# Kernel tuning notes

Hardware: AMD Instinct MI355X
Metric: run time of the kernel (lower is better)

Reference implementation:

```python
import jax, jax.numpy as jnp
import numpy as np

N_NODES = 50000
N_EDGES = 800000


def setup_inputs() -> dict:
    key = jax.random.key(0)
    ks = jax.random.split(key, 9)
    d, h, hd = 128, 4, 32
    s = 1.0 / np.sqrt(d)
    return {
        "x": jax.random.normal(ks[0], (N_NODES, d), jnp.float32),
        "edge_index": jax.random.randint(ks[1], (2, N_EDGES), 0, N_NODES, jnp.int32),
        "W0": jax.random.normal(ks[2], (d, d), jnp.float32) * s,
        "att_l0": jax.random.normal(ks[3], (h, hd), jnp.float32) * s,
        "att_r0": jax.random.normal(ks[4], (h, hd), jnp.float32) * s,
        "b0": jnp.zeros((d,), jnp.float32),
        "W1": jax.random.normal(ks[5], (d, d), jnp.float32) * s,
        "att_l1": jax.random.normal(ks[6], (h, hd), jnp.float32) * s,
        "att_r1": jax.random.normal(ks[7], (h, hd), jnp.float32) * s,
        "b1": jnp.zeros((hd,), jnp.float32),
    }


def _gat_layer(x, src, dst, W, att_l, att_r, bias, concat):
    # x: [N, F_in]; W: [H*D, F_in] (torch Linear layout); att_*: [H, D]
    n = x.shape[0]
    h, d = att_l.shape
    hx = (x @ W.T).reshape(n, h, d)                     # [N,H,D]
    al = jnp.einsum('nhd,hd->nh', hx, att_l)            # [N,H]
    ar = jnp.einsum('nhd,hd->nh', hx, att_r)
    att = al[src] + ar[dst]                             # [E,H]
    att = jax.nn.leaky_relu(att, negative_slope=0.2)
    # segment softmax over destination nodes
    m = jax.ops.segment_max(att, dst, num_segments=n)   # [N,H]
    att = jnp.exp(att - m[dst])
    ssum = jax.ops.segment_sum(att, dst, num_segments=n)
    att = att / (ssum[dst] + 1e-9)                      # [E,H]
    msgs = att[:, :, None] * hx[src]                    # [E,H,D]
    out = jax.ops.segment_sum(msgs, dst, num_segments=n)  # [N,H,D]
    if concat:
        out = out.reshape(n, h * d)
    else:
        out = out.mean(axis=1)
    return out + bias


def reference(x, edge_index, W0, att_l0, att_r0, b0, W1, att_l1, att_r1, b1):
    src, dst = edge_index[0], edge_index[1]
    x = _gat_layer(x, src, dst, W0, att_l0, att_r0, b0, concat=True)
    x = jax.nn.relu(x)  # dropout is identity in eval mode
    x = _gat_layer(x, src, dst, W1, att_l1, att_r1, b1, concat=False)
    return x
```

## Files before the change

### kernel.cpp

```cpp
#include <hip/hip_runtime.h>
#include <hip/hip_bf16.h>

#define H 4
#define D 32
#define F 128
#define MAXDEG 64
#define PF 16
#define NBUCK 256
#define BUCKW 196
#define CAP   4096
#define NABLK 128
#define GB    1563

typedef __attribute__((ext_vector_type(8))) short bf16x8;
typedef __attribute__((ext_vector_type(4))) float f32x4;

__device__ __forceinline__ short f2bf(float v) {
    __hip_bfloat16 h = __float2bfloat16(v);
    return *reinterpret_cast<short*>(&h);
}
__device__ __forceinline__ float bf2f(short s) {
    __hip_bfloat16 h = *reinterpret_cast<__hip_bfloat16*>(&s);
    return __bfloat162float(h);
}

__global__ __launch_bounds__(256)
void k_init(const float* __restrict__ W0, short* __restrict__ W0hi,
            short* __restrict__ W0lo, const float* __restrict__ W1,
            short* __restrict__ W1hi, short* __restrict__ W1lo,
            int* __restrict__ gcnt) {
    const int bid = blockIdx.x;
    const int tid = threadIdx.x;
    if (bid == 0) gcnt[tid] = 0;
    const float* W  = (bid < 4) ? W0 : W1;
    short* Whi = (bid < 4) ? W0hi : W1hi;
    short* Wlo = (bid < 4) ? W0lo : W1lo;
    const int part = bid & 3;
    const int base = part * (F * F / 4);
    for (int i = base + tid * 4; i < base + F * F / 4; i += 1024) {
        float4 v = *reinterpret_cast<const float4*>(W + i);
        float vv[4] = {v.x, v.y, v.z, v.w};
        short hs[4], ls[4];
#pragma unroll
        for (int j = 0; j < 4; ++j) {
            hs[j] = f2bf(vv[j]);
            ls[j] = f2bf(vv[j] - bf2f(hs[j]));
        }
        *reinterpret_cast<short4*>(Whi + i) = make_short4(hs[0], hs[1], hs[2], hs[3]);
        *reinterpret_cast<short4*>(Wlo + i) = make_short4(ls[0], ls[1], ls[2], ls[3]);
    }
}

__device__ __forceinline__
void bucketA_body(int abid, const int* __restrict__ ei, int E,
                  int* __restrict__ gcnt, unsigned int* __restrict__ buf) {
    __shared__ int lcnt[NBUCK];
    __shared__ int lpos[NBUCK];
    const int tid = threadIdx.x;
    lcnt[tid] = 0;
    __syncthreads();
    const int per = ((E / NABLK) + 3) & ~3;
    const int e0 = abid * per;
    const int e1 = min(e0 + per, E);
    for (int e = e0 + 4 * tid; e < e1; e += 1024) {
        int4 dv = *reinterpret_cast<const int4*>(ei + E + e);
        atomicAdd(&lcnt[dv.x / BUCKW], 1);
        atomicAdd(&lcnt[dv.y / BUCKW], 1);
        atomicAdd(&lcnt[dv.z / BUCKW], 1);
        atomicAdd(&lcnt[dv.w / BUCKW], 1);
    }
    __syncthreads();
    if (lcnt[tid] > 0)
        lpos[tid] = atomicAdd(&gcnt[tid], lcnt[tid]);
    __syncthreads();
    for (int e = e0 + 4 * tid; e < e1; e += 1024) {
        int4 sv = *reinterpret_cast<const int4*>(ei + e);
        int4 dv = *reinterpret_cast<const int4*>(ei + E + e);
        int ss[4] = {sv.x, sv.y, sv.z, sv.w};
        int dd[4] = {dv.x, dv.y, dv.z, dv.w};
#pragma unroll
        for (int j = 0; j < 4; ++j) {
            int b = dd[j] / BUCKW;
            int pos = atomicAdd(&lpos[b], 1);
            if (pos < CAP)
                buf[(size_t)b * CAP + pos] =
                    (unsigned)ss[j] | ((unsigned)(dd[j] - b * BUCKW) << 16);
        }
    }
}

__device__ __forceinline__
void bsetup_pre(const short* __restrict__ Whi, const short* __restrict__ Wlo,
                int wave, int m, int q8, bf16x8 Bhi[2][4], bf16x8 Blo[2][4]) {
#pragma unroll
    for (int j = 0; j < 2; ++j) {
        const int fout = wave * 32 + j * 16 + m;
#pragma unroll
        for (int kc = 0; kc < 4; ++kc) {
            Bhi[j][kc] = *reinterpret_cast<const bf16x8*>(Whi + (size_t)fout * F + kc * 32 + q8);
            Blo[j][kc] = *reinterpret_cast<const bf16x8*>(Wlo + (size_t)fout * F + kc * 32 + q8);
        }
    }
}

__device__ __forceinline__
void loadA_f32(const float* __restrict__ X, int node0, int m, int q8, float4 r[8]) {
    const float* xp = X + (size_t)(node0 + m) * F + q8;
#pragma unroll
    for (int kc = 0; kc < 4; ++kc) {
        r[2 * kc]     = *reinterpret_cast<const float4*>(xp + kc * 32);
        r[2 * kc + 1] = *reinterpret_cast<const float4*>(xp + kc * 32 + 4);
    }
}

__device__ __forceinline__
void splitA(const float4 r[8], bf16x8 Ahi[4], bf16x8 Alo[4]) {
#pragma unroll
    for (int kc = 0; kc < 4; ++kc) {
        float xv[8] = {r[2 * kc].x, r[2 * kc].y, r[2 * kc].z, r[2 * kc].w,
                       r[2 * kc + 1].x, r[2 * kc + 1].y, r[2 * kc + 1].z, r[2 * kc + 1].w};
#pragma unroll
        for (int t2 = 0; t2 < 8; ++t2) {
            short hh = f2bf(xv[t2]);
            Ahi[kc][t2] = hh;
            Alo[kc][t2] = f2bf(xv[t2] - bf2f(hh));
        }
    }
}

__device__ __forceinline__
void loadA_bf(const short* __restrict__ Xhi, const short* __restrict__ Xlo,
              int node0, int m, int q8, bf16x8 Ahi[4], bf16x8 Alo[4]) {
    const short* xh = Xhi + (size_t)(node0 + m) * F + q8;
    const short* xl = Xlo + (size_t)(node0 + m) * F + q8;
#pragma unroll
    for (int kc = 0; kc < 4; ++kc) {
        Ahi[kc] = *reinterpret_cast<const bf16x8*>(xh + kc * 32);
        Alo[kc] = *reinterpret_cast<const bf16x8*>(xl + kc * 32);
    }
}

__device__ __forceinline__
void mfma_epi(int tile, const bf16x8 Ahi[4], const bf16x8 Alo[4],
              const bf16x8 Bhi[2][4], const bf16x8 Blo[2][4],
              float alw0, float alw16, float arw0, float arw16,
              __hip_bfloat16* __restrict__ HXB, float* __restrict__ AL,
              float* __restrict__ AR, int wave, int m, int q) {
    const int node0 = tile * 16;
    f32x4 acc0 = {0.f, 0.f, 0.f, 0.f};
    f32x4 acc1 = {0.f, 0.f, 0.f, 0.f};
#pragma unroll
    for (int kc = 0; kc < 4; ++kc) {
        acc0 = __builtin_amdgcn_mfma_f32_16x16x32_bf16(Ahi[kc], Bhi[0][kc], acc0, 0, 0, 0);
        acc1 = __builtin_amdgcn_mfma_f32_16x16x32_bf16(Ahi[kc], Bhi[1][kc], acc1, 0, 0, 0);
        acc0 = __builtin_amdgcn_mfma_f32_16x16x32_bf16(Ahi[kc], Blo[0][kc], acc0, 0, 0, 0);
        acc1 = __builtin_amdgcn_mfma_f32_16x16x32_bf16(Ahi[kc], Blo[1][kc], acc1, 0, 0, 0);
        acc0 = __builtin_amdgcn_mfma_f32_16x16x32_bf16(Alo[kc], Bhi[0][kc], acc0, 0, 0, 0);
        acc1 = __builtin_amdgcn_mfma_f32_16x16x32_bf16(Alo[kc], Bhi[1][kc], acc1, 0, 0, 0);
    }
    const int row0 = node0 + q * 4;
    const int col0 = wave * 32 + m;
#pragma unroll
    for (int r = 0; r < 4; ++r) {
        HXB[(size_t)(row0 + r) * F + col0]      = __float2bfloat16(acc0[r]);
        HXB[(size_t)(row0 + r) * F + col0 + 16] = __float2bfloat16(acc1[r]);
        float pal = acc0[r] * alw0 + acc1[r] * alw16;
        float par = acc0[r] * arw0 + acc1[r] * arw16;
#pragma unroll
        for (int o = 1; o < 16; o <<= 1) {
            pal += __shfl_xor(pal, o);
            par += __shfl_xor(par, o);
        }
        if (m == 0) {
            AL[(size_t)(row0 + r) * H + wave] = pal;
            AR[(size_t)(row0 + r) * H + wave] = par;
        }
    }
}

__device__ __forceinline__
void gemm_pair_f32(int bid, const float* __restrict__ X,
                   const short* __restrict__ Whi, const short* __restrict__ Wlo,
                   const float* __restrict__ attl, const float* __restrict__ attr,
                   __hip_bfloat16* __restrict__ HXB, float* __restrict__ AL,
                   float* __restrict__ AR, int ntiles) {
    const int wave = threadIdx.x >> 6;
    const int lane = threadIdx.x & 63;
    const int m    = lane & 15;
    const int q    = lane >> 4;
    const int q8   = q * 8;
    bf16x8 Bhi[2][4], Blo[2][4];
    bsetup_pre(Whi, Wlo, wave, m, q8, Bhi, Blo);
    const float alw0  = attl[wave * 32 + m];
    const float alw16 = attl[wave * 32 + 16 + m];
    const float arw0  = attr[wave * 32 + m];
    const float arw16 = attr[wave * 32 + 16 + m];

    const int t0 = bid, t1 = bid + GB;
    const bool has1 = t1 < ntiles;
    float4 r0[8], r1[8];
    loadA_f32(X, t0 * 16, m, q8, r0);
    if (has1) loadA_f32(X, t1 * 16, m, q8, r1);
    bf16x8 Ahi[4], Alo[4];
    splitA(r0, Ahi, Alo);
    mfma_epi(t0, Ahi, Alo, Bhi, Blo, alw0, alw16, arw0, arw16, HXB, AL, AR, wave, m, q);
    if (has1) {
        splitA(r1, Ahi, Alo);
        mfma_epi(t1, Ahi, Alo, Bhi, Blo, alw0, alw16, arw0, arw16, HXB, AL, AR, wave, m, q);
    }
}

__device__ __forceinline__
void gemm_pair_bf(int bid, const short* __restrict__ Xhi, const short* __restrict__ Xlo,
                  const short* __restrict__ Whi, const short* __restrict__ Wlo,
                  const float* __restrict__ attl, const float* __restrict__ attr,
                  __hip_bfloat16* __restrict__ HXB, float* __restrict__ AL,
                  float* __restrict__ AR, int ntiles) {
    const int wave = threadIdx.x >> 6;
    const int lane = threadIdx.x & 63;
    const int m    = lane & 15;
    const int q    = lane >> 4;
    const int q8   = q * 8;
    bf16x8 Bhi[2][4], Blo[2][4];
    bsetup_pre(Whi, Wlo, wave, m, q8, Bhi, Blo);
    const float alw0  = attl[wave * 32 + m];
    const float alw16 = attl[wave * 32 + 16 + m];
    const float arw0  = attr[wave * 32 + m];
    const float arw16 = attr[wave * 32 + 16 + m];

    const int t0 = bid, t1 = bid + GB;
    const bool has1 = t1 < ntiles;
    bf16x8 A0h[4], A0l[4], A1h[4], A1l[4];
    loadA_bf(Xhi, Xlo, t0 * 16, m, q8, A0h, A0l);
    if (has1) loadA_bf(Xhi, Xlo, t1 * 16, m, q8, A1h, A1l);
    mfma_epi(t0, A0h, A0l, Bhi, Blo, alw0, alw16, arw0, arw16, HXB, AL, AR, wave, m, q);
    if (has1)
        mfma_epi(t1, A1h, A1l, Bhi, Blo, alw0, alw16, arw0, arw16, HXB, AL, AR, wave, m, q);
}

__global__ __launch_bounds__(256)
void k_pre(const float* __restrict__ X, const short* __restrict__ W0hi,
           const short* __restrict__ W0lo, const float* __restrict__ attl0,
           const float* __restrict__ attr0, __hip_bfloat16* __restrict__ HXB,
           float* __restrict__ AL, float* __restrict__ AR, int ntiles,
           const int* __restrict__ ei, int E,
           int* __restrict__ gcnt, unsigned int* __restrict__ buf) {
    const int bid = blockIdx.x;
    if (bid < GB)
        gemm_pair_f32(bid, X, W0hi, W0lo, attl0, attr0, HXB, AL, AR, ntiles);
    else
        bucketA_body(bid - GB, ei, E, gcnt, buf);
}

__global__ __launch_bounds__(256)
void k_bucket(const unsigned int* __restrict__ buf, const int* __restrict__ gcnt,
              int* __restrict__ deg, unsigned short* __restrict__ ssrc2u, int N) {
    __shared__ int cnt[BUCKW];
    __shared__ unsigned short slots[BUCKW * MAXDEG];
    const int b = blockIdx.x;
    const int tid = threadIdx.x;
    if (tid < BUCKW) cnt[tid] = 0;
    __syncthreads();
    const int mm = min(gcnt[b], CAP);
    const int m4 = mm & ~3;
    for (int i = 4 * tid; i < m4; i += 1024) {
        uint4 r = *reinterpret_cast<const uint4*>(buf + (size_t)b * CAP + i);
        unsigned rr[4] = {r.x, r.y, r.z, r.w};
#pragma unroll
        for (int j = 0; j < 4; ++j) {
            int src  = rr[j] & 0xffff;
            int ldst = rr[j] >> 16;
            int slot = atomicAdd(&cnt[ldst], 1);
            if (slot < MAXDEG)
                slots[ldst * MAXDEG + slot] = (unsigned short)src;
        }
    }
    for (int i = m4 + tid; i < mm; i += 256) {
        unsigned rec = buf[(size_t)b * CAP + i];
        int src  = rec & 0xffff;
        int ldst = rec >> 16;
        int slot = atomicAdd(&cnt[ldst], 1);
        if (slot < MAXDEG)
            slots[ldst * MAXDEG + slot] = (unsigned short)src;
    }
    __syncthreads();
    uint4* dst = reinterpret_cast<uint4*>(ssrc2u + (size_t)b * BUCKW * MAXDEG);
    const uint4* s4 = reinterpret_cast<const uint4*>(slots);
    for (int i = tid; i < BUCKW * MAXDEG / 8; i += 256)
        dst[i] = s4[i];
    if (tid < BUCKW) {
        int node = b * BUCKW + tid;
        if (node < N) deg[node] = cnt[tid];
    }
}

__device__ __forceinline__
int stage_node(int g, int t, int n, const unsigned short* __restrict__ ssrc2u,
               const int* __restrict__ deg, const float* __restrict__ AL,
               const float4 ar4, int (*sidx)[MAXDEG], float (*sw)[MAXDEG][H]) {
    const int cnt  = min(deg[n], MAXDEG);
    const int rcnt = (cnt + PF - 1) & ~(PF - 1);
    if (t < rcnt) {
        if (t < cnt) {
            int s = ssrc2u[(size_t)n * MAXDEG + t];
            sidx[g][t] = s;
            float4 al4 = *reinterpret_cast<const float4*>(AL + (size_t)s * H);
            float a0 = al4.x + ar4.x; a0 = a0 > 0.f ? a0 : 0.2f * a0;
            float a1 = al4.y + ar4.y; a1 = a1 > 0.f ? a1 : 0.2f * a1;
            float a2 = al4.z + ar4.z; a2 = a2 > 0.f ? a2 : 0.2f * a2;
            float a3 = al4.w + ar4.w; a3 = a3 > 0.f ? a3 : 0.2f * a3;
            sw[g][t][0] = __expf(a0);
            sw[g][t][1] = __expf(a1);
            sw[g][t][2] = __expf(a2);
            sw[g][t][3] = __expf(a3);
        } else {
            sidx[g][t] = 0;
            sw[g][t][0] = 0.f; sw[g][t][1] = 0.f; sw[g][t][2] = 0.f; sw[g][t][3] = 0.f;
        }
    }
    __builtin_amdgcn_wave_barrier();
    return rcnt;
}

__device__ __forceinline__
void gather_node(int g, int t, int h, int rcnt, const __hip_bfloat16* __restrict__ HXB,
                 const int (*sidx)[MAXDEG], const float (*sw)[MAXDEG][H],
                 float& accx, float& accy, float& wsum) {
    for (int base = 0; base < rcnt; base += PF) {
        __hip_bfloat162 v[PF];
#pragma unroll
        for (int j = 0; j < PF; ++j) {
            int s = sidx[g][base + j];
            v[j] = *reinterpret_cast<const __hip_bfloat162*>(HXB + (size_t)s * F + 2 * t);
        }
#pragma unroll
        for (int j = 0; j < PF; ++j) {
            float w = sw[g][base + j][h];
            float2 f = __bfloat1622float2(v[j]);
            accx += w * f.x;
            accy += w * f.y;
            wsum += w;
        }
    }
}

__global__ __launch_bounds__(256)
void k_aggr0(const unsigned short* __restrict__ ssrc2u, const int* __restrict__ deg,
             const float* __restrict__ AL, const float* __restrict__ AR,
             const __hip_bfloat16* __restrict__ HXB, const float* __restrict__ bias,
             short* __restrict__ X1hi, short* __restrict__ X1lo, int N) {
    __shared__ int   sidx[4][MAXDEG];
    __shared__ float sw[4][MAXDEG][H];
    const int g = threadIdx.x >> 6;
    const int t = threadIdx.x & 63;
    const int n = blockIdx.x * 4 + g;
    if (n >= N) return;
    const int h = t >> 4;
    const float4 ar4 = *reinterpret_cast<const float4*>(AR + (size_t)n * H);
    int rcnt = stage_node(g, t, n, ssrc2u, deg, AL, ar4, sidx, sw);
    float accx = 0.f, accy = 0.f, wsum = 0.f;
    gather_node(g, t, h, rcnt, HXB, sidx, sw, accx, accy, wsum);
    float inv = 1.f / (wsum + 1e-9f);
    float ox = fmaxf(accx * inv + bias[2 * t], 0.f);
    float oy = fmaxf(accy * inv + bias[2 * t + 1], 0.f);
    short h0 = f2bf(ox), h1 = f2bf(oy);
    short l0 = f2bf(ox - bf2f(h0)), l1 = f2bf(oy - bf2f(h1));
    unsigned hw = (unsigned)(unsigned short)h0 | ((unsigned)(unsigned short)h1 << 16);
    unsigned lw = (unsigned)(unsigned short)l0 | ((unsigned)(unsigned short)l1 << 16);
    *reinterpret_cast<unsigned*>(X1hi + (size_t)n * F + 2 * t) = hw;
    *reinterpret_cast<unsigned*>(X1lo + (size_t)n * F + 2 * t) = lw;
}

__global__ __launch_bounds__(256)
void k_gemm1(const short* __restrict__ X1hi, const short* __restrict__ X1lo,
             const short* __restrict__ W1hi, const short* __restrict__ W1lo,
             const float* __restrict__ attl, const float* __restrict__ attr,
             __hip_bfloat16* __restrict__ HXB, float* __restrict__ AL,
             float* __restrict__ AR, int ntiles) {
    gemm_pair_bf(blockIdx.x, X1hi, X1lo, W1hi, W1lo, attl, attr,
                 HXB, AL, AR, ntiles);
}

__global__ __launch_bounds__(256)
void k_aggr1(const unsigned short* __restrict__ ssrc2u, const int* __restrict__ deg,
             const float* __restrict__ AL, const float* __restrict__ AR,
             const __hip_bfloat16* __restrict__ HXB, const float* __restrict__ bias,
             float* __restrict__ out, int N) {
    __shared__ int   sidx[4][MAXDEG];
    __shared__ float sw[4][MAXDEG][H];
    const int g = threadIdx.x >> 6;
    const int t = threadIdx.x & 63;
    const int n = blockIdx.x * 4 + g;
    if (n >= N) return;
    const int h = t >> 4;
    const float4 ar4 = *reinterpret_cast<const float4*>(AR + (size_t)n * H);
    int rcnt = stage_node(g, t, n, ssrc2u, deg, AL, ar4, sidx, sw);
    float accx = 0.f, accy = 0.f, wsum = 0.f;
    gather_node(g, t, h, rcnt, HXB, sidx, sw, accx, accy, wsum);
    float inv = 1.f / (wsum + 1e-9f);
    float vx = accx * inv, vy = accy * inv;
    vx += __shfl_xor(vx, 16); vx += __shfl_xor(vx, 32);
    vy += __shfl_xor(vy, 16); vy += __shfl_xor(vy, 32);
    if (t < 16) {
        float2 o;
        o.x = 0.25f * vx + bias[2 * t];
        o.y = 0.25f * vy + bias[2 * t + 1];
        *reinterpret_cast<float2*>(out + (size_t)n * D + 2 * t) = o;
    }
}

extern "C" void kernel_launch(void* const* d_in, const int* in_sizes, int n_in,
                              void* d_out, int out_size, void* d_ws, size_t ws_size,
                              hipStream_t stream) {
    const float* x     = (const float*)d_in[0];
    const int*   ei    = (const int*)d_in[1];
    const float* W0    = (const float*)d_in[2];
    const float* attl0 = (const float*)d_in[3];
    const float* attr0 = (const float*)d_in[4];
    const float* b0    = (const float*)d_in[5];
    const float* W1    = (const float*)d_in[6];
    const float* attl1 = (const float*)d_in[7];
    const float* attr1 = (const float*)d_in[8];
    const float* b1    = (const float*)d_in[9];

    const int N = in_sizes[0] / F;
    const int E = in_sizes[1] / 2;
    const int ntiles = N / 16;

    char* p = (char*)d_ws;
    __hip_bfloat16* HXB = (__hip_bfloat16*)p;   p += (size_t)N * F * 2;
    short* X1hi = (short*)p;                    p += (size_t)N * F * 2;
    short* X1lo = (short*)p;                    p += (size_t)N * F * 2;
    short* W0hi = (short*)p;                    p += (size_t)F * F * 2;
    short* W0lo = (short*)p;                    p += (size_t)F * F * 2;
    short* W1hi = (short*)p;                    p += (size_t)F * F * 2;
    short* W1lo = (short*)p;                    p += (size_t)F * F * 2;
    float* AL   = (float*)p;                    p += (size_t)N * H * 4;
    float* AR   = (float*)p;                    p += (size_t)N * H * 4;
    unsigned short* ssrc2u = (unsigned short*)p;
    p += (size_t)NBUCK * BUCKW * MAXDEG * 2;
    int* deg = (int*)p;                         p += (size_t)N * 4;
    unsigned int* buf = (unsigned int*)p;       p += (size_t)NBUCK * CAP * 4;
    int* gcnt = (int*)p;

    k_init<<<8, 256, 0, stream>>>(W0, W0hi, W0lo, W1, W1hi, W1lo, gcnt);

    k_pre<<<GB + NABLK, 256, 0, stream>>>(x, W0hi, W0lo, attl0, attr0,
                                          HXB, AL, AR, ntiles, ei, E, gcnt, buf);

    k_bucket<<<NBUCK, 256, 0, stream>>>(buf, gcnt, deg, ssrc2u, N);

    k_aggr0<<<(N + 3) / 4, 256, 0, stream>>>(ssrc2u, deg, AL, AR, HXB, b0,
                                             X1hi, X1lo, N);

    k_gemm1<<<GB, 256, 0, stream>>>(X1hi, X1lo, W1hi, W1lo, attl1, attr1,
                                    HXB, AL, AR, ntiles);

    k_aggr1<<<(N + 3) / 4, 256, 0, stream>>>(ssrc2u, deg, AL, AR, HXB, b1,
                                             (float*)d_out, N);
}
```

Measured before the change: 222.9 us.

## Replace global-atomic bucket offsets with per-block fixed-size segments and count matrix

Each bucketing block now writes its edges into a private fixed-capacity segment per bucket and records its per-bucket count in a count matrix, instead of reserving ranges with global atomics on a shared counter. The bucket kernel reads the count matrix and walks the 128 segments, so the counter no longer has to be zeroed in the init kernel. This removes global atomic contention and the init dependency. Segments are padded to 16-byte chunks, which adds reads of unused slots, and a block that sends more than 64 edges to one bucket silently drops the excess.

```diff
diff --git a/kernel.cpp b/kernel.cpp
--- a/kernel.cpp
+++ b/kernel.cpp
@@ -8,8 +8,8 @@
 #define PF 16
 #define NBUCK 256
 #define BUCKW 196
-#define CAP   4096
 #define NABLK 128
+#define SEGCAP 64
 #define GB    1563
 
 typedef __attribute__((ext_vector_type(8))) short bf16x8;
@@ -27,11 +27,9 @@
 __global__ __launch_bounds__(256)
 void k_init(const float* __restrict__ W0, short* __restrict__ W0hi,
             short* __restrict__ W0lo, const float* __restrict__ W1,
-            short* __restrict__ W1hi, short* __restrict__ W1lo,
-            int* __restrict__ gcnt) {
+            short* __restrict__ W1hi, short* __restrict__ W1lo) {
     const int bid = blockIdx.x;
     const int tid = threadIdx.x;
-    if (bid == 0) gcnt[tid] = 0;
     const float* W  = (bid < 4) ? W0 : W1;
     short* Whi = (bid < 4) ? W0hi : W1hi;
     short* Wlo = (bid < 4) ? W0lo : W1lo;
@@ -53,9 +51,8 @@
 
 __device__ __forceinline__
 void bucketA_body(int abid, const int* __restrict__ ei, int E,
-                  int* __restrict__ gcnt, unsigned int* __restrict__ buf) {
+                  int* __restrict__ cntmat, unsigned int* __restrict__ buf) {
     __shared__ int lcnt[NBUCK];
-    __shared__ int lpos[NBUCK];
     const int tid = threadIdx.x;
     lcnt[tid] = 0;
     __syncthreads();
@@ -70,8 +67,8 @@
         atomicAdd(&lcnt[dv.w / BUCKW], 1);
     }
     __syncthreads();
-    if (lcnt[tid] > 0)
-        lpos[tid] = atomicAdd(&gcnt[tid], lcnt[tid]);
+    cntmat[abid * NBUCK + tid] = min(lcnt[tid], SEGCAP);
+    lcnt[tid] = 0;
     __syncthreads();
     for (int e = e0 + 4 * tid; e < e1; e += 1024) {
         int4 sv = *reinterpret_cast<const int4*>(ei + e);
@@ -81,9 +78,9 @@
 #pragma unroll
         for (int j = 0; j < 4; ++j) {
             int b = dd[j] / BUCKW;
-            int pos = atomicAdd(&lpos[b], 1);
-            if (pos < CAP)
-                buf[(size_t)b * CAP + pos] =
+            int pos = atomicAdd(&lcnt[b], 1);
+            if (pos < SEGCAP)
+                buf[((size_t)b * NABLK + abid) * SEGCAP + pos] =
                     (unsigned)ss[j] | ((unsigned)(dd[j] - b * BUCKW) << 16);
         }
     }
@@ -244,44 +241,42 @@
            const float* __restrict__ attr0, __hip_bfloat16* __restrict__ HXB,
            float* __restrict__ AL, float* __restrict__ AR, int ntiles,
            const int* __restrict__ ei, int E,
-           int* __restrict__ gcnt, unsigned int* __restrict__ buf) {
+           int* __restrict__ cntmat, unsigned int* __restrict__ buf) {
     const int bid = blockIdx.x;
     if (bid < GB)
         gemm_pair_f32(bid, X, W0hi, W0lo, attl0, attr0, HXB, AL, AR, ntiles);
     else
-        bucketA_body(bid - GB, ei, E, gcnt, buf);
-}
-
-__global__ __launch_bounds__(256)
-void k_bucket(const unsigned int* __restrict__ buf, const int* __restrict__ gcnt,
+        bucketA_body(bid - GB, ei, E, cntmat, buf);
+}
+
+__global__ __launch_bounds__(256)
+void k_bucket(const unsigned int* __restrict__ buf, const int* __restrict__ cntmat,
               int* __restrict__ deg, unsigned short* __restrict__ ssrc2u, int N) {
     __shared__ int cnt[BUCKW];
+    __shared__ int scnt[NABLK];
     __shared__ unsigned short slots[BUCKW * MAXDEG];
     const int b = blockIdx.x;
     const int tid = threadIdx.x;
     if (tid < BUCKW) cnt[tid] = 0;
+    if (tid < NABLK) scnt[tid] = cntmat[tid * NBUCK + b];
     __syncthreads();
-    const int mm = min(gcnt[b], CAP);
-    const int m4 = mm & ~3;
-    for (int i = 4 * tid; i < m4; i += 1024) {
-        uint4 r = *reinterpret_cast<const uint4*>(buf + (size_t)b * CAP + i);
+    const int a    = tid & (NABLK - 1);
+    const int half = tid >> 7;
+    const int mm   = scnt[a];
+    const unsigned int* seg = buf + ((size_t)b * NABLK + a) * SEGCAP;
+    for (int c = half * 4; c < mm; c += 8) {
+        uint4 r = *reinterpret_cast<const uint4*>(seg + c);
         unsigned rr[4] = {r.x, r.y, r.z, r.w};
 #pragma unroll
         for (int j = 0; j < 4; ++j) {
-            int src  = rr[j] & 0xffff;
-            int ldst = rr[j] >> 16;
-            int slot = atomicAdd(&cnt[ldst], 1);
-            if (slot < MAXDEG)
-                slots[ldst * MAXDEG + slot] = (unsigned short)src;
-        }
-    }
-    for (int i = m4 + tid; i < mm; i += 256) {
-        unsigned rec = buf[(size_t)b * CAP + i];
-        int src  = rec & 0xffff;
-        int ldst = rec >> 16;
-        int slot = atomicAdd(&cnt[ldst], 1);
-        if (slot < MAXDEG)
-            slots[ldst * MAXDEG + slot] = (unsigned short)src;
+            if (c + j < mm) {
+                int src  = rr[j] & 0xffff;
+                int ldst = rr[j] >> 16;
+                int slot = atomicAdd(&cnt[ldst], 1);
+                if (slot < MAXDEG)
+                    slots[ldst * MAXDEG + slot] = (unsigned short)src;
+            }
+        }
     }
     __syncthreads();
     uint4* dst = reinterpret_cast<uint4*>(ssrc2u + (size_t)b * BUCKW * MAXDEG);
@@ -440,15 +435,15 @@
     unsigned short* ssrc2u = (unsigned short*)p;
     p += (size_t)NBUCK * BUCKW * MAXDEG * 2;
     int* deg = (int*)p;                         p += (size_t)N * 4;
-    unsigned int* buf = (unsigned int*)p;       p += (size_t)NBUCK * CAP * 4;
-    int* gcnt = (int*)p;
-
-    k_init<<<8, 256, 0, stream>>>(W0, W0hi, W0lo, W1, W1hi, W1lo, gcnt);
+    unsigned int* buf = (unsigned int*)p;       p += (size_t)NBUCK * NABLK * SEGCAP * 4;
+    int* cntmat = (int*)p;
+
+    k_init<<<8, 256, 0, stream>>>(W0, W0hi, W0lo, W1, W1hi, W1lo);
 
     k_pre<<<GB + NABLK, 256, 0, stream>>>(x, W0hi, W0lo, attl0, attr0,
-                                          HXB, AL, AR, ntiles, ei, E, gcnt, buf);
-
-    k_bucket<<<NBUCK, 256, 0, stream>>>(buf, gcnt, deg, ssrc2u, N);
+                                          HXB, AL, AR, ntiles, ei, E, cntmat, buf);
+
+    k_bucket<<<NBUCK, 256, 0, stream>>>(buf, cntmat, deg, ssrc2u, N);
 
     k_aggr0<<<(N + 3) / 4, 256, 0, stream>>>(ssrc2u, deg, AL, AR, HXB, b0,
                                              X1hi, X1lo, N);
```

Measured after the change: 219.5 us. Within noise of the previous version (-1.5%).
